# Optimization experiments

Measured on AMD Instinct MI355X. Metric: run time of the kernel, lower is better.

The kernel has to match this reference:

```python
import jax, jax.numpy as jnp
import numpy as np

N = 50000      # nodes
E = 800000     # edges (avg degree 16)
H = 128        # hidden_dim
GDIM = 64      # global feature dim
G = 10         # DiffGroupNorm groups
LAMDA = 0.01
EPS = 1e-5


def setup_inputs() -> dict:
    key = jax.random.key(0)
    ks = jax.random.split(key, 24)
    s = 0.05
    inp = {
        "x": jax.random.normal(ks[0], (N, H), dtype=jnp.float32),
        "edge_index": jax.random.randint(ks[1], (2, E), 0, N, dtype=jnp.int32),
        "edge_features": jax.random.normal(ks[2], (E, H), dtype=jnp.float32),
        "global_feat": jax.random.normal(ks[3], (1, GDIM), dtype=jnp.float32),
        # combine: Dense(H) on concat [x | messages | global] -> (H+H+GDIM, H)
        "Wc": jax.random.normal(ks[4], (H + H + GDIM, H), dtype=jnp.float32) * s,
        "bc": jnp.zeros((H,), jnp.float32),
    }
    for i, tag in enumerate(["a", "b"]):
        k = jax.random.split(ks[5 + i], 4)
        inp[f"W1{tag}"] = jax.random.normal(k[0], (H, H), dtype=jnp.float32) * s
        inp[f"b1{tag}"] = jnp.zeros((H,), jnp.float32)
        inp[f"W2{tag}"] = jax.random.normal(k[1], (H, H), dtype=jnp.float32) * s
        inp[f"b2{tag}"] = jnp.zeros((H,), jnp.float32)
        inp[f"linW{tag}"] = jax.random.normal(k[2], (H, G), dtype=jnp.float32) * s
        inp[f"linb{tag}"] = jnp.zeros((G,), jnp.float32)
        inp[f"gamma{tag}"] = jnp.ones((G * H,), jnp.float32)
        inp[f"beta{tag}"] = jnp.zeros((G * H,), jnp.float32)
    return inp


def _diff_group_norm(x, linW, linb, gamma, beta):
    # DiffGroupNorm: soft group assignment + per-(group,channel) batch norm.
    n, f = x.shape
    s = jax.nn.softmax(x @ linW + linb, axis=-1)            # [N, G]
    o = (s[:, :, None] * x[:, None, :]).reshape(n, G * f)   # [N, G*F]
    mu = o.mean(axis=0)
    var = o.var(axis=0)
    o = (o - mu) * jax.lax.rsqrt(var + EPS) * gamma + beta
    return x + LAMDA * o.reshape(n, G, f).sum(axis=1)


def _block(out, W1, b1, W2, b2, linW, linb, gamma, beta):
    h = jax.nn.softplus(out @ W1 + b1) @ W2 + b2
    h = _diff_group_norm(h, linW, linb, gamma, beta)
    return out + h


def reference(x, edge_index, edge_features, global_feat, Wc, bc,
              W1a, b1a, W2a, b2a, linWa, linba, gammaa, betaa,
              W1b, b1b, W2b, b2b, linWb, linbb, gammab, betab):
    n = x.shape[0]
    row = edge_index[0]
    # tf.scatter_nd accumulates duplicates -> segment sum over destination nodes
    messages = jax.ops.segment_sum(edge_features, row, num_segments=n)
    g = jnp.repeat(global_feat, n // global_feat.shape[0], axis=0)
    combined = jnp.concatenate([x, messages, g], axis=-1)
    out = jax.nn.softplus(combined @ Wc + bc)
    initial = out
    out = _block(out, W1a, b1a, W2a, b2a, linWa, linba, gammaa, betaa)
    out = _block(out, W1b, b1b, W2b, b2b, linWb, linbb, gammab, betab)
    return out + initial
```

## Files before the change

kernel.cpp:

```cpp
#include <hip/hip_runtime.h>
#include <math.h>

constexpr int NN = 50000;
constexpr int NE = 800000;
constexpr int HD = 128;
constexpr int NG = 10;
constexpr float LAM = 0.01f;
constexpr float EPSV = 1e-5f;
constexpr int NBLK = (NN + 255) / 256;
constexpr int GBLK = (NN + 63) / 64;

typedef __attribute__((ext_vector_type(8))) short s8v;
typedef __attribute__((ext_vector_type(4))) float f4v;

constexpr int SMEM_BYTES = 76864;

__device__ __forceinline__ float softplus_f(float x) {
    return fmaxf(x, 0.f) + log1pf(expf(-fabsf(x)));
}
__device__ __forceinline__ unsigned short f2b(float f) {
    unsigned u = __float_as_uint(f);
    unsigned r = (u + 0x7FFFu + ((u >> 16) & 1u)) >> 16;
    return (unsigned short)r;
}
__device__ __forceinline__ float b2f(unsigned short u) {
    return __uint_as_float(((unsigned)u) << 16);
}

__global__ __launch_bounds__(256) void hist_kernel(
    const int* __restrict__ rows, int* __restrict__ cnt)
{
    int base = (blockIdx.x * 256 + threadIdx.x) * 4;
    if (base < NE) {
        int4 r = *reinterpret_cast<const int4*>(rows + base);
        atomicAdd(&cnt[r.x], 1);
        atomicAdd(&cnt[r.y], 1);
        atomicAdd(&cnt[r.z], 1);
        atomicAdd(&cnt[r.w], 1);
    }
}

__global__ __launch_bounds__(256) void scan1_kernel(
    const int* __restrict__ cnt, int* __restrict__ bsum)
{
    __shared__ int red[256];
    int t = threadIdx.x;
    int i = blockIdx.x * 256 + t;
    red[t] = (i < NN) ? cnt[i] : 0;
    __syncthreads();
    for (int d = 128; d > 0; d >>= 1) {
        if (t < d) red[t] += red[t + d];
        __syncthreads();
    }
    if (t == 0) bsum[blockIdx.x] = red[0];
}

__global__ __launch_bounds__(256) void scan3_kernel(
    const int* __restrict__ cnt, const int* __restrict__ bsum,
    int* __restrict__ off, int* __restrict__ cur)
{
    __shared__ int sh[256];
    __shared__ int bs[256];
    __shared__ int basev;
    int t = threadIdx.x;
    int i = blockIdx.x * 256 + t;
    int v  = (i < NN) ? cnt[i] : 0;
    int bv = (t < NBLK) ? bsum[t] : 0;
    sh[t] = v; bs[t] = bv;
    __syncthreads();
    for (int d = 1; d < 256; d <<= 1) {
        int u1 = (t >= d) ? sh[t - d] : 0;
        int u2 = (t >= d) ? bs[t - d] : 0;
        __syncthreads();
        sh[t] += u1; bs[t] += u2;
        __syncthreads();
    }
    if (t == (int)blockIdx.x) basev = bs[t] - bv;
    __syncthreads();
    int excl = sh[t] - v + basev;
    if (i < NN) { off[i] = excl; cur[i] = excl; }
    if (i == NN - 1) off[NN] = NE;
}

__global__ __launch_bounds__(256) void fill_kernel(
    const int* __restrict__ rows, int* __restrict__ cur, int* __restrict__ eid)
{
    int base = (blockIdx.x * 256 + threadIdx.x) * 4;
    if (base < NE) {
        int4 r = *reinterpret_cast<const int4*>(rows + base);
        eid[atomicAdd(&cur[r.x], 1)] = base + 0;
        eid[atomicAdd(&cur[r.y], 1)] = base + 1;
        eid[atomicAdd(&cur[r.z], 1)] = base + 2;
        eid[atomicAdd(&cur[r.w], 1)] = base + 3;
    }
}

__global__ __launch_bounds__(256) void gather_kernel(
    const float* __restrict__ ef, const int* __restrict__ off,
    const int* __restrict__ eid, uint2* __restrict__ msgbf)
{
    int node = blockIdx.x * 4 + (threadIdx.x >> 6);
    if (node >= NN) return;
    int lane = threadIdx.x & 63;
    int half = lane >> 5, lc = lane & 31;
    int b = off[node], e = off[node + 1];
    float4 acc = make_float4(0.f, 0.f, 0.f, 0.f);
    for (int i = b + half; i < e; i += 2) {
        int ed = eid[i];
        float4 v = *reinterpret_cast<const float4*>(ef + (size_t)ed * HD + lc * 4);
        acc.x += v.x; acc.y += v.y; acc.z += v.z; acc.w += v.w;
    }
    acc.x += __shfl_xor(acc.x, 32);
    acc.y += __shfl_xor(acc.y, 32);
    acc.z += __shfl_xor(acc.z, 32);
    acc.w += __shfl_xor(acc.w, 32);
    if (half == 0) {
        uint2 pk;
        pk.x = (unsigned)f2b(acc.x) | ((unsigned)f2b(acc.y) << 16);
        pk.y = (unsigned)f2b(acc.z) | ((unsigned)f2b(acc.w) << 16);
        msgbf[(size_t)node * 32 + lc] = pk;
    }
}

__global__ __launch_bounds__(256) void prep_kernel(
    const float* __restrict__ Wc,
    const float* __restrict__ W1a, const float* __restrict__ W2a,
    const float* __restrict__ W1b, const float* __restrict__ W2b,
    short* __restrict__ wct, short* __restrict__ wts)
{
    int i = blockIdx.x * 256 + threadIdx.x;
    if (i < 40960) {
        int n = i / 320, kk = i % 320;
        wct[i] = (short)f2b(Wc[kk * 128 + n]);
    } else if (i < 40960 + 4 * 16384) {
        int j = i - 40960;
        int mat = j >> 14;
        int idx = j & 16383;
        int n = idx >> 7, kk = idx & 127;
        const float* src = (mat == 0) ? W1a : (mat == 1) ? W2a : (mat == 2) ? W1b : W2b;
        wts[j] = (short)f2b(src[kk * 128 + n]);
    }
}

__device__ __forceinline__ void fused12_tail(
    char* smem, const short* __restrict__ w2t,
    unsigned short* __restrict__ hbf, float* __restrict__ sout,
    float* __restrict__ sums, int m0)
{
    short* As = (short*)(smem);
    short* Ws = (short*)(smem + 17408);
    short* Ts = (short*)(smem + 52224);
    float* b1s = (float*)(smem + 69632);
    float* b2s = (float*)(smem + 70144);
    float* lws = (float*)(smem + 70656);
    float* lbs = (float*)(smem + 76288);
    float* hF = (float*)(smem);
    float* sS = (float*)(smem + 33792);

    const int tid = threadIdx.x;
    const int lane = tid & 63;
    const int wv = tid >> 6;
    const int fr = lane & 15;
    const int fc = lane >> 4;

    f4v acc[8];
    #pragma unroll
    for (int ct = 0; ct < 8; ++ct) acc[ct] = (f4v){0.f, 0.f, 0.f, 0.f};
    {
        const short* ap = As + (wv * 16 + fr) * 136 + fc * 8;
        const short* bp = Ws + fr * 136 + fc * 8;
        #pragma unroll
        for (int ks = 0; ks < 4; ++ks) {
            s8v a = *(const s8v*)(ap + ks * 32);
            #pragma unroll
            for (int ct = 0; ct < 8; ++ct) {
                s8v b = *(const s8v*)(bp + ct * 16 * 136 + ks * 32);
                acc[ct] = __builtin_amdgcn_mfma_f32_16x16x32_bf16(a, b, acc[ct], 0, 0, 0);
            }
        }
    }
    {
        int rb = wv * 16 + fc * 4;
        #pragma unroll
        for (int ct = 0; ct < 8; ++ct) {
            int col = ct * 16 + fr;
            float bv = b1s[col];
            #pragma unroll
            for (int r = 0; r < 4; ++r)
                Ts[(rb + r) * 136 + col] = (short)f2b(softplus_f(acc[ct][r] + bv));
        }
    }
    __syncthreads();
    {
        int col = tid >> 1, seg = (tid & 1) * 64;
        const short* src = w2t + (size_t)col * 128 + seg;
        #pragma unroll
        for (int j = 0; j < 8; ++j)
            *(s8v*)&Ws[col * 136 + seg + 8 * j] = *(const s8v*)(src + 8 * j);
    }
    __syncthreads();

    #pragma unroll
    for (int ct = 0; ct < 8; ++ct) acc[ct] = (f4v){0.f, 0.f, 0.f, 0.f};
    {
        const short* ap = Ts + (wv * 16 + fr) * 136 + fc * 8;
        const short* bp = Ws + fr * 136 + fc * 8;
        #pragma unroll
        for (int ks = 0; ks < 4; ++ks) {
            s8v a = *(const s8v*)(ap + ks * 32);
            #pragma unroll
            for (int ct = 0; ct < 8; ++ct) {
                s8v b = *(const s8v*)(bp + ct * 16 * 136 + ks * 32);
                acc[ct] = __builtin_amdgcn_mfma_f32_16x16x32_bf16(a, b, acc[ct], 0, 0, 0);
            }
        }
    }
    #pragma unroll
    for (int ct = 0; ct < 8; ++ct) {
        float bv = b2s[ct * 16 + fr];
        #pragma unroll
        for (int r = 0; r < 4; ++r) acc[ct][r] += bv;
    }
    float dot[4][10];
    #pragma unroll
    for (int r = 0; r < 4; ++r)
        #pragma unroll
        for (int g = 0; g < 10; ++g) dot[r][g] = 0.f;
    #pragma unroll
    for (int ct = 0; ct < 8; ++ct) {
        #pragma unroll
        for (int g = 0; g < 10; ++g) {
            float lwv = lws[(ct * 16 + fr) * 11 + g];
            #pragma unroll
            for (int r = 0; r < 4; ++r) dot[r][g] += acc[ct][r] * lwv;
        }
    }
    #pragma unroll
    for (int r = 0; r < 4; ++r)
        #pragma unroll
        for (int g = 0; g < 10; ++g) {
            float v = dot[r][g];
            v += __shfl_xor(v, 1);
            v += __shfl_xor(v, 2);
            v += __shfl_xor(v, 4);
            v += __shfl_xor(v, 8);
            dot[r][g] = v + lbs[g];
        }
    #pragma unroll
    for (int r = 0; r < 4; ++r) {
        float m = dot[r][0];
        #pragma unroll
        for (int g = 1; g < 10; ++g) m = fmaxf(m, dot[r][g]);
        float sum = 0.f;
        #pragma unroll
        for (int g = 0; g < 10; ++g) { dot[r][g] = expf(dot[r][g] - m); sum += dot[r][g]; }
        float inv = 1.f / sum;
        #pragma unroll
        for (int g = 0; g < 10; ++g) dot[r][g] *= inv;
    }
    const int growb = m0 + wv * 16 + fc * 4;
    const int rlocb = wv * 16 + fc * 4;
    unsigned short hq[8][4];
    #pragma unroll
    for (int ct = 0; ct < 8; ++ct) {
        int col = ct * 16 + fr;
        #pragma unroll
        for (int r = 0; r < 4; ++r) {
            hq[ct][r] = f2b(acc[ct][r]);
            int row = growb + r;
            if (row < NN) hbf[(size_t)row * 128 + col] = hq[ct][r];
        }
    }
    if (fr < 10) {
        #pragma unroll
        for (int r = 0; r < 4; ++r) {
            int row = growb + r;
            if (row < NN) {
                float v = 0.f;
                #pragma unroll
                for (int g = 0; g < 10; ++g) v = (fr == g) ? dot[r][g] : v;
                sout[(size_t)row * 10 + fr] = v;
            }
        }
    }
    __syncthreads();
    #pragma unroll
    for (int ct = 0; ct < 8; ++ct) {
        int col = ct * 16 + fr;
        #pragma unroll
        for (int r = 0; r < 4; ++r) {
            bool valid = (growb + r) < NN;
            hF[(rlocb + r) * 132 + col] = valid ? b2f(hq[ct][r]) : 0.f;
        }
    }
    if (fr < 10) {
        #pragma unroll
        for (int r = 0; r < 4; ++r) {
            bool valid = (growb + r) < NN;
            float v = 0.f;
            #pragma unroll
            for (int g = 0; g < 10; ++g) v = (fr == g) ? dot[r][g] : v;
            sS[(rlocb + r) * 10 + fr] = valid ? v : 0.f;
        }
    }
    __syncthreads();
    {
        const int c = tid & 127;
        const int g0 = (tid >> 7) * 5;
        float a1[5], a2[5];
        #pragma unroll
        for (int q = 0; q < 5; ++q) { a1[q] = 0.f; a2[q] = 0.f; }
        for (int n = 0; n < 64; ++n) {
            float hv = hF[n * 132 + c];
            #pragma unroll
            for (int q = 0; q < 5; ++q) {
                float pv = sS[n * 10 + g0 + q] * hv;
                a1[q] += pv;
                a2[q] += pv * pv;
            }
        }
        #pragma unroll
        for (int q = 0; q < 5; ++q) {
            atomicAdd(&sums[(g0 + q) * 128 + c], a1[q]);
            atomicAdd(&sums[1280 + (g0 + q) * 128 + c], a2[q]);
        }
    }
}

__global__ __launch_bounds__(256) void combine_f12a_kernel(
    const float* __restrict__ x, const short* __restrict__ msgbf,
    const float* __restrict__ gf, const short* __restrict__ wct,
    const float* __restrict__ bc,
    const short* __restrict__ w1t, const short* __restrict__ w2t,
    const float* __restrict__ b1, const float* __restrict__ b2,
    const float* __restrict__ linW, const float* __restrict__ linb,
    unsigned short* __restrict__ out0bf, unsigned short* __restrict__ hbf,
    float* __restrict__ sout, float* __restrict__ sums)
{
    __shared__ __align__(16) char smem[SMEM_BYTES];
    short* cAs = (short*)(smem);
    short* cWs = (short*)(smem + 9216);
    short* As  = (short*)(smem);
    short* Ws  = (short*)(smem + 17408);
    float* b1s = (float*)(smem + 69632);
    float* b2s = (float*)(smem + 70144);
    float* lws = (float*)(smem + 70656);
    float* lbs = (float*)(smem + 76288);
    float* bcs = (float*)(smem + 76352);

    const int tid = threadIdx.x;
    const int m0 = blockIdx.x * 64;
    if (tid < 128) { bcs[tid] = bc[tid]; b1s[tid] = b1[tid]; b2s[tid] = b2[tid]; }
    for (int i = tid; i < 1280; i += 256) lws[(i / 10) * 11 + (i % 10)] = linW[i];
    if (tid < 10) lbs[tid] = linb[tid];
    const int lane = tid & 63;
    const int wv = tid >> 6;
    const int fr = lane & 15;
    const int fc = lane >> 4;

    f4v acc[8];
    #pragma unroll
    for (int ct = 0; ct < 8; ++ct) acc[ct] = (f4v){0.f, 0.f, 0.f, 0.f};

    const int arow = tid >> 2;
    const int aseg = (tid & 3) * 16;
    const int wcol = tid >> 1;
    const int wseg = (tid & 1) * 32;

    for (int c = 0; c < 5; ++c) {
        const int k0 = c * 64;
        {
            short tmp[16];
            int grow = m0 + arow;
            if (grow >= NN) {
                #pragma unroll
                for (int j = 0; j < 16; ++j) tmp[j] = 0;
            } else if (c < 2) {
                const float* src = x + (size_t)grow * 128 + k0 + aseg;
                #pragma unroll
                for (int q = 0; q < 4; ++q) {
                    float4 v = *reinterpret_cast<const float4*>(src + 4 * q);
                    tmp[4*q+0] = (short)f2b(v.x); tmp[4*q+1] = (short)f2b(v.y);
                    tmp[4*q+2] = (short)f2b(v.z); tmp[4*q+3] = (short)f2b(v.w);
                }
            } else if (c < 4) {
                const short* src = msgbf + (size_t)grow * 128 + (k0 - 128) + aseg;
                *(s8v*)tmp = *(const s8v*)src;
                *(s8v*)(tmp + 8) = *(const s8v*)(src + 8);
            } else {
                const float* src = gf + aseg;
                #pragma unroll
                for (int q = 0; q < 4; ++q) {
                    float4 v = *reinterpret_cast<const float4*>(src + 4 * q);
                    tmp[4*q+0] = (short)f2b(v.x); tmp[4*q+1] = (short)f2b(v.y);
                    tmp[4*q+2] = (short)f2b(v.z); tmp[4*q+3] = (short)f2b(v.w);
                }
            }
            *(s8v*)&cAs[arow * 72 + aseg] = *(s8v*)tmp;
            *(s8v*)&cAs[arow * 72 + aseg + 8] = *(s8v*)(tmp + 8);
        }
        {
            const short* src = wct + (size_t)wcol * 320 + k0 + wseg;
            #pragma unroll
            for (int j = 0; j < 4; ++j)
                *(s8v*)&cWs[wcol * 72 + wseg + 8 * j] = *(const s8v*)(src + 8 * j);
        }
        __syncthreads();
        const short* ap = cAs + (wv * 16 + fr) * 72 + fc * 8;
        const short* bp = cWs + fr * 72 + fc * 8;
        #pragma unroll
        for (int ks = 0; ks < 2; ++ks) {
            s8v a = *(const s8v*)(ap + ks * 32);
            #pragma unroll
            for (int ct = 0; ct < 8; ++ct) {
                s8v b = *(const s8v*)(bp + ct * 16 * 72 + ks * 32);
                acc[ct] = __builtin_amdgcn_mfma_f32_16x16x32_bf16(a, b, acc[ct], 0, 0, 0);
            }
        }
        __syncthreads();
    }
    const int rbase = m0 + wv * 16 + fc * 4;
    const int rloc  = wv * 16 + fc * 4;
    #pragma unroll
    for (int ct = 0; ct < 8; ++ct) {
        int col = ct * 16 + fr;
        float bv = bcs[col];
        #pragma unroll
        for (int r = 0; r < 4; ++r) {
            unsigned short q = f2b(softplus_f(acc[ct][r] + bv));
            bool valid = (rbase + r) < NN;
            if (valid) out0bf[(size_t)(rbase + r) * 128 + col] = q;
            As[(rloc + r) * 136 + col] = valid ? (short)q : (short)0;
        }
    }
    {
        int col = tid >> 1, seg = (tid & 1) * 64;
        const short* src = w1t + (size_t)col * 128 + seg;
        #pragma unroll
        for (int j = 0; j < 8; ++j)
            *(s8v*)&Ws[col * 136 + seg + 8 * j] = *(const s8v*)(src + 8 * j);
    }
    __syncthreads();
    fused12_tail(smem, w2t, hbf, sout, sums, m0);
}

__global__ __launch_bounds__(256) void apply_f12b_kernel(
    const unsigned short* __restrict__ out0bf,
    const float* __restrict__ sums_a,
    const float* __restrict__ gamma_a, const float* __restrict__ beta_a,
    const short* __restrict__ w1t, const short* __restrict__ w2t,
    const float* __restrict__ b1, const float* __restrict__ b2,
    const float* __restrict__ linW, const float* __restrict__ linb,
    unsigned short* __restrict__ out1bf,
    unsigned short* __restrict__ hbf,
    float* __restrict__ sout,
    float* __restrict__ sums_b)
{
    __shared__ __align__(16) char smem[SMEM_BYTES];
    float* ws_  = (float*)(smem);
    float* mus_ = (float*)(smem + 5120);
    float* ks_  = (float*)(smem + 10240);
    float* ss_  = (float*)(smem + 10752);
    short* As   = (short*)(smem);
    short* Ws   = (short*)(smem + 17408);
    float* b1s  = (float*)(smem + 69632);
    float* b2s  = (float*)(smem + 70144);
    float* lws  = (float*)(smem + 70656);
    float* lbs  = (float*)(smem + 76288);

    const int tid = threadIdx.x;
    const int m0 = blockIdx.x * 64;
    if (tid < 128) { b1s[tid] = b1[tid]; b2s[tid] = b2[tid]; }
    for (int i = tid; i < 1280; i += 256) lws[(i / 10) * 11 + (i % 10)] = linW[i];
    if (tid < 10) lbs[tid] = linb[tid];
    const float invn = 1.f / (float)NN;
    for (int idx = tid; idx < 1280; idx += 256) {
        float s1 = sums_a[idx], s2 = sums_a[idx + 1280];
        float mu = s1 * invn;
        float var = s2 * invn - mu * mu;
        float wg = rsqrtf(var + EPSV) * gamma_a[idx];
        ws_[idx] = wg;
        mus_[idx] = mu;
    }
    for (int i = tid; i < 640; i += 256) {
        int n = m0 + i / 10;
        ss_[i] = (n < NN) ? sout[(size_t)n * 10 + i % 10] : 0.f;
    }
    {
        int col = tid >> 1, seg = (tid & 1) * 64;
        const short* src = w1t + (size_t)col * 128 + seg;
        #pragma unroll
        for (int j = 0; j < 8; ++j)
            *(s8v*)&Ws[col * 136 + seg + 8 * j] = *(const s8v*)(src + 8 * j);
    }
    __syncthreads();
    if (tid < 128) {
        float kacc = 0.f;
        #pragma unroll
        for (int g = 0; g < NG; ++g) {
            int idx = g * 128 + tid;
            kacc += beta_a[idx] - mus_[idx] * ws_[idx];
        }
        ks_[tid] = kacc;
    }
    __syncthreads();
    const int tc = tid & 31, rg = tid >> 5;
    ushort4 vals[8];
    #pragma unroll
    for (int p = 0; p < 8; ++p) {
        int nl = p * 8 + rg;
        int n = m0 + nl;
        if (n >= NN) { vals[p].x = vals[p].y = vals[p].z = vals[p].w = 0; continue; }
        float A0 = 0.f, A1 = 0.f, A2 = 0.f, A3 = 0.f;
        #pragma unroll
        for (int g = 0; g < 10; ++g) {
            float sv = ss_[nl * 10 + g];
            float4 wv4 = *reinterpret_cast<const float4*>(&ws_[g * 128 + tc * 4]);
            A0 += sv * wv4.x; A1 += sv * wv4.y; A2 += sv * wv4.z; A3 += sv * wv4.w;
        }
        ushort4 hv4 = *reinterpret_cast<const ushort4*>(hbf + (size_t)n * 128 + tc * 4);
        ushort4 ov4 = *reinterpret_cast<const ushort4*>(out0bf + (size_t)n * 128 + tc * 4);
        float h0 = b2f(hv4.x), h1 = b2f(hv4.y), h2 = b2f(hv4.z), h3 = b2f(hv4.w);
        float r0 = b2f(ov4.x) + h0 + LAM * (h0 * A0 + ks_[tc * 4 + 0]);
        float r1 = b2f(ov4.y) + h1 + LAM * (h1 * A1 + ks_[tc * 4 + 1]);
        float r2 = b2f(ov4.z) + h2 + LAM * (h2 * A2 + ks_[tc * 4 + 2]);
        float r3 = b2f(ov4.w) + h3 + LAM * (h3 * A3 + ks_[tc * 4 + 3]);
        ushort4 o;
        o.x = f2b(r0); o.y = f2b(r1); o.z = f2b(r2); o.w = f2b(r3);
        *reinterpret_cast<ushort4*>(out1bf + (size_t)n * 128 + tc * 4) = o;
        vals[p] = o;
    }
    __syncthreads();
    #pragma unroll
    for (int p = 0; p < 8; ++p) {
        int row = p * 8 + rg;
        *reinterpret_cast<ushort4*>(&As[row * 136 + tc * 4]) = vals[p];
    }
    __syncthreads();
    fused12_tail(smem, w2t, hbf, sout, sums_b, m0);
}

__global__ __launch_bounds__(256) void apply_last_kernel(
    const unsigned short* __restrict__ out1bf,
    const unsigned short* __restrict__ hbf,
    const float* __restrict__ s, const float* __restrict__ sums,
    const float* __restrict__ gamma, const float* __restrict__ beta,
    const unsigned short* __restrict__ out0bf,
    float* __restrict__ dstf)
{
    __shared__ __align__(16) float ws_[1280];
    __shared__ float mus_[1280];
    __shared__ float ks_[128];
    __shared__ float ss_[640];
    const int tid = threadIdx.x;
    const int m0 = blockIdx.x * 64;
    const float invn = 1.f / (float)NN;
    for (int idx = tid; idx < 1280; idx += 256) {
        float s1 = sums[idx], s2 = sums[idx + 1280];
        float mu = s1 * invn;
        float var = s2 * invn - mu * mu;
        float wg = rsqrtf(var + EPSV) * gamma[idx];
        ws_[idx] = wg;
        mus_[idx] = mu;
    }
    for (int i = tid; i < 640; i += 256) {
        int n = m0 + i / 10;
        ss_[i] = (n < NN) ? s[(size_t)n * 10 + i % 10] : 0.f;
    }
    __syncthreads();
    if (tid < 128) {
        float kacc = 0.f;
        #pragma unroll
        for (int g = 0; g < NG; ++g) {
            int idx = g * 128 + tid;
            kacc += beta[idx] - mus_[idx] * ws_[idx];
        }
        ks_[tid] = kacc;
    }
    __syncthreads();
    const int tc = tid & 31, rg = tid >> 5;
    #pragma unroll
    for (int p = 0; p < 8; ++p) {
        int nl = p * 8 + rg;
        int n = m0 + nl;
        if (n >= NN) continue;
        float A0 = 0.f, A1 = 0.f, A2 = 0.f, A3 = 0.f;
        #pragma unroll
        for (int g = 0; g < 10; ++g) {
            float sv = ss_[nl * 10 + g];
            float4 wv4 = *reinterpret_cast<const float4*>(&ws_[g * 128 + tc * 4]);
            A0 += sv * wv4.x; A1 += sv * wv4.y; A2 += sv * wv4.z; A3 += sv * wv4.w;
        }
        ushort4 hv4 = *reinterpret_cast<const ushort4*>(hbf + (size_t)n * 128 + tc * 4);
        ushort4 ov4 = *reinterpret_cast<const ushort4*>(out1bf + (size_t)n * 128 + tc * 4);
        ushort4 iv4 = *reinterpret_cast<const ushort4*>(out0bf + (size_t)n * 128 + tc * 4);
        float h0 = b2f(hv4.x), h1 = b2f(hv4.y), h2 = b2f(hv4.z), h3 = b2f(hv4.w);
        float r0 = b2f(ov4.x) + h0 + LAM * (h0 * A0 + ks_[tc * 4 + 0]) + b2f(iv4.x);
        float r1 = b2f(ov4.y) + h1 + LAM * (h1 * A1 + ks_[tc * 4 + 1]) + b2f(iv4.y);
        float r2 = b2f(ov4.z) + h2 + LAM * (h2 * A2 + ks_[tc * 4 + 2]) + b2f(iv4.z);
        float r3 = b2f(ov4.w) + h3 + LAM * (h3 * A3 + ks_[tc * 4 + 3]) + b2f(iv4.w);
        *reinterpret_cast<float4*>(dstf + (size_t)n * 128 + tc * 4) =
            make_float4(r0, r1, r2, r3);
    }
}

extern "C" void kernel_launch(void* const* d_in, const int* in_sizes, int n_in,
                              void* d_out, int out_size, void* d_ws, size_t ws_size,
                              hipStream_t stream)
{
    const float* x    = (const float*)d_in[0];
    const int*   eidx = (const int*)  d_in[1];
    const float* ef   = (const float*)d_in[2];
    const float* gf   = (const float*)d_in[3];
    const float* Wc   = (const float*)d_in[4];
    const float* bc   = (const float*)d_in[5];

    float* p = (float*)d_ws;
    int*   cnt    = (int*)p;                      p += NN;
    float* sums_a = p;                            p += 2560;
    float* sums_b = p;                            p += 2560;
    unsigned short* msgbf  = (unsigned short*)p;  p += (size_t)NN * 64;
    unsigned short* out0bf = (unsigned short*)p;  p += (size_t)NN * 64;
    unsigned short* out1bf = (unsigned short*)p;  p += (size_t)NN * 64;
    unsigned short* hbf    = (unsigned short*)p;  p += (size_t)NN * 64;
    float* sbuf = p;                              p += (size_t)NN * 10;
    short* wct  = (short*)p;
    short* wts  = wct + 40960;

    int* off   = (int*)out1bf;
    int* cur   = off + NN + 1;
    int* bsum  = cur + NN;
    int* eid   = (int*)hbf;

    prep_kernel<<<416, 256, 0, stream>>>(
        Wc, (const float*)d_in[6], (const float*)d_in[8],
        (const float*)d_in[14], (const float*)d_in[16], wct, wts);

    hipMemsetAsync(cnt, 0, sizeof(int) * (NN + 2 * 2560), stream);

    const int eblocks = (NE / 4 + 255) / 256;
    hist_kernel <<<eblocks, 256, 0, stream>>>(eidx, cnt);
    scan1_kernel<<<NBLK, 256, 0, stream>>>(cnt, bsum);
    scan3_kernel<<<NBLK, 256, 0, stream>>>(cnt, bsum, off, cur);
    fill_kernel <<<eblocks, 256, 0, stream>>>(eidx, cur, eid);
    gather_kernel<<<(NN + 3) / 4, 256, 0, stream>>>(ef, off, eid, (uint2*)msgbf);

    const short* w1ta = wts;
    const short* w2ta = wts + 16384;
    const short* w1tb = wts + 32768;
    const short* w2tb = wts + 49152;

    combine_f12a_kernel<<<GBLK, 256, 0, stream>>>(
        x, (const short*)msgbf, gf, wct, bc,
        w1ta, w2ta, (const float*)d_in[7], (const float*)d_in[9],
        (const float*)d_in[10], (const float*)d_in[11],
        out0bf, hbf, sbuf, sums_a);

    apply_f12b_kernel<<<GBLK, 256, 0, stream>>>(
        out0bf, sums_a, (const float*)d_in[12], (const float*)d_in[13],
        w1tb, w2tb, (const float*)d_in[15], (const float*)d_in[17],
        (const float*)d_in[18], (const float*)d_in[19],
        out1bf, hbf, sbuf, sums_b);

    apply_last_kernel<<<GBLK, 256, 0, stream>>>(
        out1bf, hbf, sbuf, sums_b, (const float*)d_in[20], (const float*)d_in[21],
        out0bf, (float*)d_out);
}
```

Before: 416.4 us.

## Merge weight prep into histogram, widen gather loads, replicate norm stat accumulators

After: 397.3 us. 1.05x faster.

```diff
diff --git a/kernel.cpp b/kernel.cpp
--- a/kernel.cpp
+++ b/kernel.cpp
@@ -9,6 +9,7 @@
 constexpr float EPSV = 1e-5f;
 constexpr int NBLK = (NN + 255) / 256;
 constexpr int GBLK = (NN + 63) / 64;
+constexpr int NCOPY = 8;
 
 typedef __attribute__((ext_vector_type(8))) short s8v;
 typedef __attribute__((ext_vector_type(4))) float f4v;
@@ -27,16 +28,37 @@
     return __uint_as_float(((unsigned)u) << 16);
 }
 
-__global__ __launch_bounds__(256) void hist_kernel(
-    const int* __restrict__ rows, int* __restrict__ cnt)
-{
-    int base = (blockIdx.x * 256 + threadIdx.x) * 4;
-    if (base < NE) {
-        int4 r = *reinterpret_cast<const int4*>(rows + base);
-        atomicAdd(&cnt[r.x], 1);
-        atomicAdd(&cnt[r.y], 1);
-        atomicAdd(&cnt[r.z], 1);
-        atomicAdd(&cnt[r.w], 1);
+constexpr int EBLOCKS = (NE / 4 + 255) / 256;
+__global__ __launch_bounds__(256) void hist_prep_kernel(
+    const int* __restrict__ rows, int* __restrict__ cnt,
+    const float* __restrict__ Wc,
+    const float* __restrict__ W1a, const float* __restrict__ W2a,
+    const float* __restrict__ W1b, const float* __restrict__ W2b,
+    short* __restrict__ wct, short* __restrict__ wts)
+{
+    if ((int)blockIdx.x < EBLOCKS) {
+        int base = (blockIdx.x * 256 + threadIdx.x) * 4;
+        if (base < NE) {
+            int4 r = *reinterpret_cast<const int4*>(rows + base);
+            atomicAdd(&cnt[r.x], 1);
+            atomicAdd(&cnt[r.y], 1);
+            atomicAdd(&cnt[r.z], 1);
+            atomicAdd(&cnt[r.w], 1);
+        }
+    } else {
+        int i = (blockIdx.x - EBLOCKS) * 256 + threadIdx.x;
+        if (i < 40960) {
+            int n = i / 320, kk = i % 320;
+            wct[i] = (short)f2b(Wc[kk * 128 + n]);
+        } else if (i < 40960 + 4 * 16384) {
+            int j = i - 40960;
+            int mat = j >> 14;
+            int idx = j & 16383;
+            int n = idx >> 7, kk = idx & 127;
+            const float* src = (mat == 0) ? W1a : (mat == 1) ? W2a
+                             : (mat == 2) ? W1b : W2b;
+            wts[j] = (short)f2b(src[kk * 128 + n]);
+        }
     }
 }
 
@@ -97,55 +119,44 @@
 
 __global__ __launch_bounds__(256) void gather_kernel(
     const float* __restrict__ ef, const int* __restrict__ off,
-    const int* __restrict__ eid, uint2* __restrict__ msgbf)
+    const int* __restrict__ eid, uint4* __restrict__ msgbf)
 {
     int node = blockIdx.x * 4 + (threadIdx.x >> 6);
     if (node >= NN) return;
     int lane = threadIdx.x & 63;
-    int half = lane >> 5, lc = lane & 31;
+    int eg = lane >> 4;
+    int lc = lane & 15;
     int b = off[node], e = off[node + 1];
-    float4 acc = make_float4(0.f, 0.f, 0.f, 0.f);
-    for (int i = b + half; i < e; i += 2) {
+    float acc[8];
+    #pragma unroll
+    for (int j = 0; j < 8; ++j) acc[j] = 0.f;
+    for (int i = b + eg; i < e; i += 4) {
         int ed = eid[i];
-        float4 v = *reinterpret_cast<const float4*>(ef + (size_t)ed * HD + lc * 4);
-        acc.x += v.x; acc.y += v.y; acc.z += v.z; acc.w += v.w;
-    }
-    acc.x += __shfl_xor(acc.x, 32);
-    acc.y += __shfl_xor(acc.y, 32);
-    acc.z += __shfl_xor(acc.z, 32);
-    acc.w += __shfl_xor(acc.w, 32);
-    if (half == 0) {
-        uint2 pk;
-        pk.x = (unsigned)f2b(acc.x) | ((unsigned)f2b(acc.y) << 16);
-        pk.y = (unsigned)f2b(acc.z) | ((unsigned)f2b(acc.w) << 16);
-        msgbf[(size_t)node * 32 + lc] = pk;
-    }
-}
-
-__global__ __launch_bounds__(256) void prep_kernel(
-    const float* __restrict__ Wc,
-    const float* __restrict__ W1a, const float* __restrict__ W2a,
-    const float* __restrict__ W1b, const float* __restrict__ W2b,
-    short* __restrict__ wct, short* __restrict__ wts)
-{
-    int i = blockIdx.x * 256 + threadIdx.x;
-    if (i < 40960) {
-        int n = i / 320, kk = i % 320;
-        wct[i] = (short)f2b(Wc[kk * 128 + n]);
-    } else if (i < 40960 + 4 * 16384) {
-        int j = i - 40960;
-        int mat = j >> 14;
-        int idx = j & 16383;
-        int n = idx >> 7, kk = idx & 127;
-        const float* src = (mat == 0) ? W1a : (mat == 1) ? W2a : (mat == 2) ? W1b : W2b;
-        wts[j] = (short)f2b(src[kk * 128 + n]);
+        const float* src = ef + (size_t)ed * HD + lc * 8;
+        float4 v0 = *reinterpret_cast<const float4*>(src);
+        float4 v1 = *reinterpret_cast<const float4*>(src + 4);
+        acc[0] += v0.x; acc[1] += v0.y; acc[2] += v0.z; acc[3] += v0.w;
+        acc[4] += v1.x; acc[5] += v1.y; acc[6] += v1.z; acc[7] += v1.w;
+    }
+    #pragma unroll
+    for (int j = 0; j < 8; ++j) {
+        acc[j] += __shfl_xor(acc[j], 16);
+        acc[j] += __shfl_xor(acc[j], 32);
+    }
+    if (eg == 0) {
+        uint4 pk;
+        pk.x = (unsigned)f2b(acc[0]) | ((unsigned)f2b(acc[1]) << 16);
+        pk.y = (unsigned)f2b(acc[2]) | ((unsigned)f2b(acc[3]) << 16);
+        pk.z = (unsigned)f2b(acc[4]) | ((unsigned)f2b(acc[5]) << 16);
+        pk.w = (unsigned)f2b(acc[6]) | ((unsigned)f2b(acc[7]) << 16);
+        msgbf[(size_t)node * 16 + lc] = pk;
     }
 }
 
 __device__ __forceinline__ void fused12_tail(
     char* smem, const short* __restrict__ w2t,
     unsigned short* __restrict__ hbf, float* __restrict__ sout,
-    float* __restrict__ sums, int m0)
+    float* __restrict__ sums_base, int m0)
 {
     short* As = (short*)(smem);
     short* Ws = (short*)(smem + 17408);
@@ -305,6 +316,7 @@
     }
     __syncthreads();
     {
+        float* sums = sums_base + (size_t)(blockIdx.x & (NCOPY - 1)) * 2560;
         const int c = tid & 127;
         const int g0 = (tid >> 7) * 5;
         float a1[5], a2[5];
@@ -475,7 +487,12 @@
     if (tid < 10) lbs[tid] = linb[tid];
     const float invn = 1.f / (float)NN;
     for (int idx = tid; idx < 1280; idx += 256) {
-        float s1 = sums_a[idx], s2 = sums_a[idx + 1280];
+        float s1 = 0.f, s2 = 0.f;
+        #pragma unroll
+        for (int k = 0; k < NCOPY; ++k) {
+            s1 += sums_a[(size_t)k * 2560 + idx];
+            s2 += sums_a[(size_t)k * 2560 + idx + 1280];
+        }
         float mu = s1 * invn;
         float var = s2 * invn - mu * mu;
         float wg = rsqrtf(var + EPSV) * gamma_a[idx];
@@ -556,7 +573,12 @@
     const int m0 = blockIdx.x * 64;
     const float invn = 1.f / (float)NN;
     for (int idx = tid; idx < 1280; idx += 256) {
-        float s1 = sums[idx], s2 = sums[idx + 1280];
+        float s1 = 0.f, s2 = 0.f;
+        #pragma unroll
+        for (int k = 0; k < NCOPY; ++k) {
+            s1 += sums[(size_t)k * 2560 + idx];
+            s2 += sums[(size_t)k * 2560 + idx + 1280];
+        }
         float mu = s1 * invn;
         float var = s2 * invn - mu * mu;
         float wg = rsqrtf(var + EPSV) * gamma[idx];
@@ -617,8 +639,8 @@
 
     float* p = (float*)d_ws;
     int*   cnt    = (int*)p;                      p += NN;
-    float* sums_a = p;                            p += 2560;
-    float* sums_b = p;                            p += 2560;
+    float* sums_a = p;                            p += (size_t)NCOPY * 2560;
+    float* sums_b = p;                            p += (size_t)NCOPY * 2560;
     unsigned short* msgbf  = (unsigned short*)p;  p += (size_t)NN * 64;
     unsigned short* out0bf = (unsigned short*)p;  p += (size_t)NN * 64;
     unsigned short* out1bf = (unsigned short*)p;  p += (size_t)NN * 64;
@@ -632,18 +654,16 @@
     int* bsum  = cur + NN;
     int* eid   = (int*)hbf;
 
-    prep_kernel<<<416, 256, 0, stream>>>(
-        Wc, (const float*)d_in[6], (const float*)d_in[8],
+    hipMemsetAsync(cnt, 0, sizeof(int) * (NN + 2 * NCOPY * 2560), stream);
+
+    hist_prep_kernel<<<EBLOCKS + 416, 256, 0, stream>>>(
+        eidx, cnt, Wc, (const float*)d_in[6], (const float*)d_in[8],
         (const float*)d_in[14], (const float*)d_in[16], wct, wts);
 
-    hipMemsetAsync(cnt, 0, sizeof(int) * (NN + 2 * 2560), stream);
-
-    const int eblocks = (NE / 4 + 255) / 256;
-    hist_kernel <<<eblocks, 256, 0, stream>>>(eidx, cnt);
     scan1_kernel<<<NBLK, 256, 0, stream>>>(cnt, bsum);
     scan3_kernel<<<NBLK, 256, 0, stream>>>(cnt, bsum, off, cur);
-    fill_kernel <<<eblocks, 256, 0, stream>>>(eidx, cur, eid);
-    gather_kernel<<<(NN + 3) / 4, 256, 0, stream>>>(ef, off, eid, (uint2*)msgbf);
+    fill_kernel <<<EBLOCKS, 256, 0, stream>>>(eidx, cur, eid);
+    gather_kernel<<<(NN + 3) / 4, 256, 0, stream>>>(ef, off, eid, (uint4*)msgbf);
 
     const short* w1ta = wts;
     const short* w2ta = wts + 16384;
```
